# Kernel optimization log

Measured on AMD Instinct MI355X. Metric: run time of the kernel, lower is better.

The kernel has to match this reference:

```python
import jax, jax.numpy as jnp
import numpy as np

KNN, D, CONV_NUM, LEVELS, POOL_RATIO = 4, 64, 6, 3, 8
QN, RFN, NS, H, W = 4, 32, 4, 64, 64
CN = LEVELS * CONV_NUM  # 18 = 3 embed levels x 6 correlation variants


def instance_norm(x, eps=1e-5):
    # InstanceNorm2d(affine=False): normalize each (sample, channel) over H,W (biased var)
    m = x.mean(axis=(-2, -1), keepdims=True)
    v = x.var(axis=(-2, -1), keepdims=True)
    return (x - m) * jax.lax.rsqrt(v + eps)


def conv2d(x, w, b):
    y = jax.lax.conv_general_dilated(x, w, (1, 1), 'SAME', dimension_numbers=('NCHW', 'OIHW', 'NCHW'))
    return y + b[None, :, None, None]


def conv1x1x1(x, w, b):
    # Conv3d kernel 1x1x1 == pure channel mixing; x: (qn,C,ns,h,w), w: (Cout,Cin)
    return jnp.einsum('qcshw,oc->qoshw', x, w) + b[None, :, None, None, None]


def head(x, w1, b1, w2, b2, w3, b3):
    x = jax.nn.relu(conv2d(x, w1, b1))
    x = jax.nn.relu(conv2d(x, w2, b2))
    return conv2d(x, w3, b3)


def setup_inputs():
    key = jax.random.key(0)
    ks = iter(jax.random.split(key, 64))
    def rn(shape, scale=0.05):
        return jax.random.normal(next(ks), shape, jnp.float32) * scale
    inp = {'corr': jax.random.normal(next(ks), (QN, RFN, NS, CN, H, W), jnp.float32)}
    inp['scale_conv_w1'] = rn((D, CN * KNN)); inp['scale_conv_b1'] = rn((D,))
    inp['scale_conv_w2'] = rn((D, D)); inp['scale_conv_b2'] = rn((D,))
    inp['score_conv_w1'] = rn((D, LEVELS * KNN)); inp['score_conv_b1'] = rn((D,))
    inp['score_conv_w2'] = rn((D, D)); inp['score_conv_b2'] = rn((D,))
    for name, cout in (('scale_pred', 1), ('offset_pred', 2), ('score_pred', 1)):
        inp[name + '_w1'] = rn((D, D, 3, 3)); inp[name + '_b1'] = rn((D,))
        inp[name + '_w2'] = rn((D, D, 3, 3)); inp[name + '_b2'] = rn((D,))
        inp[name + '_w3'] = rn((cout, D, 3, 3)); inp[name + '_b3'] = rn((cout,))
    return inp


def _maps(corr, scale_conv_w1, scale_conv_b1, scale_conv_w2, scale_conv_b2,
          score_conv_w1, score_conv_b1, score_conv_w2, score_conv_b2,
          scale_pred_w1, scale_pred_b1, scale_pred_w2, scale_pred_b2, scale_pred_w3, scale_pred_b3,
          offset_pred_w1, offset_pred_b1, offset_pred_w2, offset_pred_b2, offset_pred_w3, offset_pred_b3,
          score_pred_w1, score_pred_b1, score_pred_w2, score_pred_b2, score_pred_w3, score_pred_b3):
    qn, rfn, ns, cn, h, w = corr.shape
    corr_n = instance_norm(corr)                         # score_norm
    # per-(scale,position) matching score per reference -> knn refs
    ref_score = corr_n.mean(axis=3)                      # qn,rfn,ns,h,w
    rs = jnp.moveaxis(ref_score, 1, -1)                  # qn,ns,h,w,rfn
    _, top_idx = jax.lax.top_k(rs, KNN)                  # qn,ns,h,w,knn
    feat = jnp.transpose(corr_n, (0, 2, 4, 5, 1, 3))     # qn,ns,h,w,rfn,cn
    knn_feat = jnp.take_along_axis(feat, top_idx[..., None], axis=4)  # qn,ns,h,w,knn,cn
    x_scale = jnp.transpose(knn_feat.reshape(qn, ns, h, w, KNN * cn), (0, 4, 1, 2, 3))  # qn,72,ns,h,w
    lvl = corr_n.reshape(qn, rfn, ns, LEVELS, CONV_NUM, h, w).mean(axis=4)  # per-level score
    lvl = jnp.transpose(lvl, (0, 2, 4, 5, 1, 3))         # qn,ns,h,w,rfn,3
    knn_lvl = jnp.take_along_axis(lvl, top_idx[..., None], axis=4)
    x_score = jnp.transpose(knn_lvl.reshape(qn, ns, h, w, KNN * LEVELS), (0, 4, 1, 2, 3))  # qn,12,ns,h,w
    xs = conv1x1x1(jax.nn.relu(conv1x1x1(x_scale, scale_conv_w1, scale_conv_b1)), scale_conv_w2, scale_conv_b2).max(axis=2)
    xc = conv1x1x1(jax.nn.relu(conv1x1x1(x_score, score_conv_w1, score_conv_b1)), score_conv_w2, score_conv_b2).max(axis=2)
    scales = head(xs, scale_pred_w1, scale_pred_b1, scale_pred_w2, scale_pred_b2, scale_pred_w3, scale_pred_b3)
    offsets = head(xc, offset_pred_w1, offset_pred_b1, offset_pred_w2, offset_pred_b2, offset_pred_w3, offset_pred_b3)
    scores = head(xc, score_pred_w1, score_pred_b1, score_pred_w2, score_pred_b2, score_pred_w3, score_pred_b3)
    return scores, scales, offsets


def reference(corr, scale_conv_w1, scale_conv_b1, scale_conv_w2, scale_conv_b2,
              score_conv_w1, score_conv_b1, score_conv_w2, score_conv_b2,
              scale_pred_w1, scale_pred_b1, scale_pred_w2, scale_pred_b2, scale_pred_w3, scale_pred_b3,
              offset_pred_w1, offset_pred_b1, offset_pred_w2, offset_pred_b2, offset_pred_w3, offset_pred_b3,
              score_pred_w1, score_pred_b1, score_pred_w2, score_pred_b2, score_pred_w3, score_pred_b3):
    scores, scales, offsets = _maps(corr, scale_conv_w1, scale_conv_b1, scale_conv_w2, scale_conv_b2,
                                    score_conv_w1, score_conv_b1, score_conv_w2, score_conv_b2,
                                    scale_pred_w1, scale_pred_b1, scale_pred_w2, scale_pred_b2, scale_pred_w3, scale_pred_b3,
                                    offset_pred_w1, offset_pred_b1, offset_pred_w2, offset_pred_b2, offset_pred_w3, offset_pred_b3,
                                    score_pred_w1, score_pred_b1, score_pred_w2, score_pred_b2, score_pred_w3, score_pred_b3)
    # parse_detection: argmax + advanced-index gathers
    qn = scores.shape[0]; h, w = scores.shape[-2:]
    sid = jnp.argmax(scores.reshape(qn, -1), axis=1)
    sy, sx = sid // w, sid % w
    q = jnp.arange(qn)
    off = offsets[q, :, sy, sx]                          # qn,2
    pos = (jnp.stack([sx, sy], -1).astype(scores.dtype) + off + 0.5) * POOL_RATIO - 0.5
    scl = 2.0 ** scales[q, 0, sy, sx]
    return pos, scl, scores, scales, offsets
```

## Files before the change

kernel.cpp:

```cpp
#include <hip/hip_runtime.h>

#define HW 4096

__global__ __launch_bounds__(256) void k_stats(const float* __restrict__ corr,
                                               float* __restrict__ scl,
                                               float* __restrict__ shf) {
  int g = blockIdx.x;
  const float4* p = (const float4*)(corr + (size_t)g * HW);
  int t = threadIdx.x;
  float s = 0.f, s2 = 0.f;
#pragma unroll
  for (int i = 0; i < 4; i++) {
    float4 v = p[t + i * 256];
    s += v.x + v.y + v.z + v.w;
    s2 += v.x * v.x + v.y * v.y + v.z * v.z + v.w * v.w;
  }
#pragma unroll
  for (int o = 32; o > 0; o >>= 1) {
    s += __shfl_down(s, o, 64);
    s2 += __shfl_down(s2, o, 64);
  }
  __shared__ float ls[4], ls2[4];
  int wid = t >> 6;
  if ((t & 63) == 0) { ls[wid] = s; ls2[wid] = s2; }
  __syncthreads();
  if (t == 0) {
    float S = ls[0] + ls[1] + ls[2] + ls[3];
    float S2 = ls2[0] + ls2[1] + ls2[2] + ls2[3];
    float m = S * (1.f / HW);
    float var = S2 * (1.f / HW) - m * m;
    float r = rsqrtf(var + 1e-5f);
    scl[g] = r;
    shf[g] = -m * r;
  }
}

__global__ __launch_bounds__(256) void k_wx(
    const float* __restrict__ p0, const float* __restrict__ p1,
    const float* __restrict__ p2, const float* __restrict__ p3,
    const float* __restrict__ p4, const float* __restrict__ p5,
    float* __restrict__ wT, const float* __restrict__ w1s,
    const float* __restrict__ w2s, const float* __restrict__ w1c,
    const float* __restrict__ w2c, float* __restrict__ wm) {
  int b = blockIdx.x;
  int t = threadIdx.x;
  if (b < 96) {
    int arr = b >> 4;
    int chunk = b & 15;
    const float* src = (arr == 0) ? p0
                       : (arr == 1) ? p1
                       : (arr == 2) ? p2
                       : (arr == 3) ? p3
                       : (arr == 4) ? p4 : p5;
    float* dst = wT + arr * 36864;
#pragma unroll
    for (int i = 0; i < 9; i++) {
      int e = chunk * 2304 + i * 256 + t;
      int oc = e / 576;
      int rem = e - oc * 576;
      dst[rem * 64 + oc] = src[e];
    }
  } else {
    int i = (b - 96) * 256 + t;
    if (i < 4608) {
      int c = i >> 6, o = i & 63;
      wm[i] = w1s[o * 72 + c];
    } else if (i < 8704) {
      int j = i - 4608;
      int c = j >> 6, o = j & 63;
      wm[i] = w2s[o * 64 + c];
    } else if (i < 9472) {
      int j = i - 8704;
      int c = j >> 6, o = j & 63;
      wm[i] = w1c[o * 12 + c];
    } else if (i < 13568) {
      int j = i - 9472;
      int c = j >> 6, o = j & 63;
      wm[i] = w2c[o * 64 + c];
    }
  }
}

__global__ __launch_bounds__(256) void k_refscore(const float* __restrict__ corr,
                                                  const float* __restrict__ scl,
                                                  const float* __restrict__ shf,
                                                  float* __restrict__ rs) {
  int b = blockIdx.x;
  int grp = b >> 2;
  int i4 = (b & 3) * 256 + threadIdx.x;
  const float* base = corr + (size_t)grp * 18 * HW;
  float4 acc = make_float4(0.f, 0.f, 0.f, 0.f);
  float sh = 0.f;
#pragma unroll
  for (int c = 0; c < 18; c++) {
    float s = scl[grp * 18 + c];
    sh += shf[grp * 18 + c];
    float4 v = ((const float4*)(base + c * HW))[i4];
    acc.x += v.x * s; acc.y += v.y * s; acc.z += v.z * s; acc.w += v.w * s;
  }
  const float inv = 1.f / 18.f;
  float4 o;
  o.x = (acc.x + sh) * inv; o.y = (acc.y + sh) * inv;
  o.z = (acc.z + sh) * inv; o.w = (acc.w + sh) * inv;
  ((float4*)(rs + (size_t)grp * HW))[i4] = o;
}

__global__ __launch_bounds__(256) void k_topk(const float* __restrict__ rs,
                                              int* __restrict__ topidx) {
  __shared__ float st[32 * 256];
  int b = blockIdx.x;
  int pxc = b & 15;
  int ns = (b >> 4) & 3;
  int q = b >> 6;
  int t = threadIdx.x;
  int pxb = pxc * 256;
#pragma unroll 8
  for (int r = 0; r < 32; r++)
    st[r * 256 + t] = rs[((q * 32 + r) * 4 + ns) * HW + pxb + t];
  __syncthreads();
  float v[32];
#pragma unroll
  for (int r = 0; r < 32; r++) v[r] = st[r * 256 + t];
  unsigned mask = 0;
  int sel[4];
#pragma unroll
  for (int k = 0; k < 4; k++) {
    float best = -3.4e38f;
    int bi = 0;
#pragma unroll
    for (int r = 0; r < 32; r++) {
      bool take = (!(mask & (1u << r))) && (v[r] > best);
      best = take ? v[r] : best;
      bi = take ? r : bi;
    }
    sel[k] = bi;
    mask |= (1u << bi);
  }
  ((int4*)topidx)[(q * 4 + ns) * HW + pxb + t] =
      make_int4(sel[0], sel[1], sel[2], sel[3]);
}

__global__ __launch_bounds__(256) void k_gather(const float* __restrict__ corr,
                                                const float* __restrict__ scl,
                                                const float* __restrict__ shf,
                                                const int* __restrict__ topidx,
                                                float* __restrict__ vbuf) {
  __shared__ float ls[32], lsh[32];
  int b = blockIdx.x;
  int c = b % 18;
  int rest = b / 18;
  int ns = rest & 3;
  int pxc = (rest >> 2) & 15;
  int q = rest >> 6;
  int t = threadIdx.x;
  int px = pxc * 256 + t;

  if (t < 32) {
    int g = q * 2304 + t * 72 + ns * 18 + c;
    ls[t] = scl[g];
    lsh[t] = shf[g];
  }
  int4 ti = ((const int4*)topidx)[(q * 4 + ns) * HW + px];
  int rk0 = ti.x, rk1 = ti.y, rk2 = ti.z, rk3 = ti.w;
  __syncthreads();

  const float* base = corr + (size_t)(((q * 32) * 4 + ns) * 18 + c) * HW + px;
  float v0 = 0.f, v1 = 0.f, v2 = 0.f, v3 = 0.f;
#pragma unroll
  for (int r = 0; r < 32; r++) {
    float x = base[(size_t)r * 72 * HW];
    v0 = (rk0 == r) ? x : v0;
    v1 = (rk1 == r) ? x : v1;
    v2 = (rk2 == r) ? x : v2;
    v3 = (rk3 == r) ? x : v3;
  }
  v0 = v0 * ls[rk0] + lsh[rk0];
  v1 = v1 * ls[rk1] + lsh[rk1];
  v2 = v2 * ls[rk2] + lsh[rk2];
  v3 = v3 * ls[rk3] + lsh[rk3];
  size_t ob = (size_t)((q * 4 + ns) * 72 + c) * HW + px;
  vbuf[ob] = v0;
  vbuf[ob + 18 * HW] = v1;
  vbuf[ob + 36 * HW] = v2;
  vbuf[ob + 54 * HW] = v3;
}

__global__ __launch_bounds__(256) void k_mlps(const float* __restrict__ vbuf,
                                              const float* __restrict__ w1T,
                                              const float* __restrict__ b1,
                                              const float* __restrict__ w2T,
                                              const float* __restrict__ b2,
                                              float* __restrict__ xs) {
  __shared__ float red8[8 * 256];
  int blk = blockIdx.x;
  int q = blk >> 6, pxc = blk & 63;
  int t = threadIdx.x;
  int ns = t >> 6;
  int lane = t & 63;
  int px = pxc * 64 + lane;

  float v[72];
  const float* vb = vbuf + (size_t)((q * 4 + ns) * 72) * HW + px;
#pragma unroll
  for (int j = 0; j < 72; j++) v[j] = vb[(size_t)j * HW];

  float h[64];
#pragma unroll
  for (int o = 0; o < 64; o++) h[o] = b1[o];
#pragma unroll 4
  for (int c = 0; c < 72; c++) {
    float x = v[c];
    const float* wr = w1T + c * 64;
#pragma unroll
    for (int o = 0; o < 64; o++) h[o] = fmaf(wr[o], x, h[o]);
  }
#pragma unroll
  for (int o = 0; o < 64; o++) h[o] = fmaxf(h[o], 0.f);
  float a[64];
#pragma unroll
  for (int o = 0; o < 64; o++) a[o] = b2[o];
#pragma unroll 4
  for (int c = 0; c < 64; c++) {
    float x = h[c];
    const float* wr = w2T + c * 64;
#pragma unroll
    for (int o = 0; o < 64; o++) a[o] = fmaf(wr[o], x, a[o]);
  }
#pragma unroll
  for (int og = 0; og < 8; og++) {
#pragma unroll
    for (int j = 0; j < 8; j++) red8[j * 256 + t] = a[og * 8 + j];
    __syncthreads();
#pragma unroll
    for (int jj = 0; jj < 2; jj++) {
      int j2 = ns * 2 + jj;
      float m = red8[j2 * 256 + lane];
#pragma unroll
      for (int n2 = 1; n2 < 4; n2++)
        m = fmaxf(m, red8[j2 * 256 + n2 * 64 + lane]);
      xs[(size_t)(q * 64 + og * 8 + j2) * HW + px] = m;
    }
    __syncthreads();
  }
}

__global__ __launch_bounds__(256) void k_mlpc(const float* __restrict__ vbuf,
                                              const float* __restrict__ w1T,
                                              const float* __restrict__ b1,
                                              const float* __restrict__ w2T,
                                              const float* __restrict__ b2,
                                              float* __restrict__ xc) {
  __shared__ float red8[8 * 256];
  int blk = blockIdx.x;
  int q = blk >> 6, pxc = blk & 63;
  int t = threadIdx.x;
  int ns = t >> 6;
  int lane = t & 63;
  int px = pxc * 64 + lane;

  float xsc[12];
  const float* vb = vbuf + (size_t)((q * 4 + ns) * 72) * HW + px;
#pragma unroll
  for (int k = 0; k < 4; k++)
#pragma unroll
    for (int l = 0; l < 3; l++) {
      float s = 0.f;
#pragma unroll
      for (int j = 0; j < 6; j++)
        s += vb[(size_t)(k * 18 + l * 6 + j) * HW];
      xsc[k * 3 + l] = s * (1.f / 6.f);
    }
  float h[64];
#pragma unroll
  for (int o = 0; o < 64; o++) h[o] = b1[o];
#pragma unroll 4
  for (int c = 0; c < 12; c++) {
    float x = xsc[c];
    const float* wr = w1T + c * 64;
#pragma unroll
    for (int o = 0; o < 64; o++) h[o] = fmaf(wr[o], x, h[o]);
  }
#pragma unroll
  for (int o = 0; o < 64; o++) h[o] = fmaxf(h[o], 0.f);
  float a[64];
#pragma unroll
  for (int o = 0; o < 64; o++) a[o] = b2[o];
#pragma unroll 4
  for (int c = 0; c < 64; c++) {
    float x = h[c];
    const float* wr = w2T + c * 64;
#pragma unroll
    for (int o = 0; o < 64; o++) a[o] = fmaf(wr[o], x, a[o]);
  }
#pragma unroll
  for (int og = 0; og < 8; og++) {
#pragma unroll
    for (int j = 0; j < 8; j++) red8[j * 256 + t] = a[og * 8 + j];
    __syncthreads();
#pragma unroll
    for (int jj = 0; jj < 2; jj++) {
      int j2 = ns * 2 + jj;
      float m = red8[j2 * 256 + lane];
#pragma unroll
      for (int n2 = 1; n2 < 4; n2++)
        m = fmaxf(m, red8[j2 * 256 + n2 * 64 + lane]);
      xc[(size_t)(q * 64 + og * 8 + j2) * HW + px] = m;
    }
    __syncthreads();
  }
}

template <bool RELU>
__global__ __launch_bounds__(256) void k_conv3h(
    const float* __restrict__ in0, const float* __restrict__ in1,
    const float* __restrict__ in2, const float* __restrict__ w0,
    const float* __restrict__ w1, const float* __restrict__ w2,
    const float* __restrict__ bb0, const float* __restrict__ bb1,
    const float* __restrict__ bb2, float* __restrict__ o0,
    float* __restrict__ o1, float* __restrict__ o2) {
  __shared__ float tile[16 * 10 * 72];
  int b = blockIdx.x;
  int hi = b >> 5;
  int og = hi / 3;
  int head = hi - og * 3;
  int q = (b >> 3) & 3;
  int rt = b & 7;
  const float* in = head == 0 ? in0 : head == 1 ? in1 : in2;
  const float* wT = head == 0 ? w0 : head == 1 ? w1 : w2;
  const float* bb = head == 0 ? bb0 : head == 1 ? bb1 : bb2;
  float* outp = head == 0 ? o0 : head == 1 ? o1 : o2;

  int t = threadIdx.x;
  int w = t & 63;
  int wr = t >> 6;
  int lane4 = t & 15;
  int rgrp = t >> 4;
  float acc[2][8];
#pragma unroll
  for (int pr = 0; pr < 2; pr++)
#pragma unroll
    for (int o = 0; o < 8; o++) acc[pr][o] = 0.f;
  const float* inq = in + (size_t)q * 64 * HW;

  for (int icc = 0; icc < 4; icc++) {
    __syncthreads();
    if (t < 160) { tile[t * 72 + 3] = 0.f; tile[t * 72 + 68] = 0.f; }
#pragma unroll
    for (int p = 0; p < 10; p++) {
      int idx = p * 16 + rgrp;
      int ch = idx / 10;
      int r = idx - ch * 10;
      int grow = rt * 8 + r - 1;
      float4 val = make_float4(0.f, 0.f, 0.f, 0.f);
      if (grow >= 0 && grow < 64)
        val = *(const float4*)(inq + (size_t)(icc * 16 + ch) * HW + grow * 64 +
                               lane4 * 4);
      *(float4*)(tile + idx * 72 + 4 + lane4 * 4) = val;
    }
    __syncthreads();
#pragma unroll 2
    for (int ic = 0; ic < 16; ic++) {
      float xv[4][3];
      const float* tb = tile + (ic * 10 + wr * 2) * 72 + w + 3;
#pragma unroll
      for (int rr = 0; rr < 4; rr++)
#pragma unroll
        for (int dc = 0; dc < 3; dc++) xv[rr][dc] = tb[rr * 72 + dc];
      const float* wb = wT + (size_t)(icc * 16 + ic) * 9 * 64 + og * 8;
#pragma unroll
      for (int dr = 0; dr < 3; dr++)
#pragma unroll
        for (int dc = 0; dc < 3; dc++) {
          const float* wv = wb + (dr * 3 + dc) * 64;
#pragma unroll
          for (int o = 0; o < 8; o++) {
            float wj = wv[o];
            acc[0][o] = fmaf(wj, xv[0 + dr][dc], acc[0][o]);
            acc[1][o] = fmaf(wj, xv[1 + dr][dc], acc[1][o]);
          }
        }
    }
  }
#pragma unroll
  for (int pr = 0; pr < 2; pr++) {
    int orow = rt * 8 + wr * 2 + pr;
#pragma unroll
    for (int o = 0; o < 8; o++) {
      float rz = acc[pr][o] + bb[og * 8 + o];
      if (RELU) rz = fmaxf(rz, 0.f);
      outp[((size_t)q * 64 + og * 8 + o) * HW + orow * 64 + w] = rz;
    }
  }
}

__global__ __launch_bounds__(256) void k_convSh(
    const float* __restrict__ in0, const float* __restrict__ in1,
    const float* __restrict__ in2, const float* __restrict__ wt0,
    const float* __restrict__ wt1, const float* __restrict__ wt2,
    const float* __restrict__ bb0, const float* __restrict__ bb1,
    const float* __restrict__ bb2, float* __restrict__ o0,
    float* __restrict__ o1, float* __restrict__ o2) {
  __shared__ float tile[64 * 3 * 66];
  __shared__ float red[4 * 2 * 64];
  int b = blockIdx.x;
  int head = b >> 8;
  int q = (b >> 6) & 3;
  int row = b & 63;
  const float* in = head == 0 ? in0 : head == 1 ? in1 : in2;
  const float* wt = head == 0 ? wt0 : head == 1 ? wt1 : wt2;
  const float* bb = head == 0 ? bb0 : head == 1 ? bb1 : bb2;
  float* outp = head == 0 ? o0 : head == 1 ? o1 : o2;
  int noc = (head == 1) ? 2 : 1;

  int t = threadIdx.x;
  int w = t & 63;
  int sub = t >> 6;
  if (t < 192) { tile[t * 66] = 0.f; tile[t * 66 + 65] = 0.f; }
  __syncthreads();
  const float* inq = in + (size_t)q * 64 * HW;
#pragma unroll
  for (int i = 0; i < 48; i++) {
    int idx = i * 4 + sub;
    int ic = idx / 3;
    int r = idx - ic * 3;
    int grow = row + r - 1;
    float val = 0.f;
    if (grow >= 0 && grow < 64) val = inq[(size_t)ic * HW + grow * 64 + w];
    tile[idx * 66 + 1 + w] = val;
  }
  __syncthreads();
  float acc0 = 0.f, acc1 = 0.f;
#pragma unroll 4
  for (int i = 0; i < 16; i++) {
    int ic = sub * 16 + i;
    float x[9];
#pragma unroll
    for (int dr = 0; dr < 3; dr++)
#pragma unroll
      for (int dc = 0; dc < 3; dc++)
        x[dr * 3 + dc] = tile[(ic * 3 + dr) * 66 + w + dc];
    const float* wb = wt + (size_t)ic * 9;
#pragma unroll
    for (int j = 0; j < 9; j++) acc0 += wb[j] * x[j];
    if (noc == 2) {
      const float* wb1 = wt + 576 + (size_t)ic * 9;
#pragma unroll
      for (int j = 0; j < 9; j++) acc1 += wb1[j] * x[j];
    }
  }
  red[(sub * 2 + 0) * 64 + w] = acc0;
  if (noc == 2) red[(sub * 2 + 1) * 64 + w] = acc1;
  __syncthreads();
  if (t < 128) {
    int o = t >> 6;
    if (o < noc) {
      float s = red[(0 * 2 + o) * 64 + w] + red[(1 * 2 + o) * 64 + w] +
                red[(2 * 2 + o) * 64 + w] + red[(3 * 2 + o) * 64 + w] + bb[o];
      outp[((size_t)q * noc + o) * HW + row * 64 + w] = s;
    }
  }
}

__global__ __launch_bounds__(256) void k_final(const float* __restrict__ scores,
                                               const float* __restrict__ scales,
                                               const float* __restrict__ offsets,
                                               float* __restrict__ pos,
                                               float* __restrict__ sclo) {
  int q = blockIdx.x, t = threadIdx.x;
  float best = -3.4e38f;
  int bi = 1 << 30;
  for (int i = t; i < HW; i += 256) {
    float v = scores[q * HW + i];
    if (v > best) { best = v; bi = i; }
  }
  __shared__ float bv[256];
  __shared__ int bix[256];
  bv[t] = best;
  bix[t] = bi;
  __syncthreads();
  for (int s = 128; s > 0; s >>= 1) {
    if (t < s) {
      if (bv[t + s] > bv[t] || (bv[t + s] == bv[t] && bix[t + s] < bix[t])) {
        bv[t] = bv[t + s];
        bix[t] = bix[t + s];
      }
    }
    __syncthreads();
  }
  if (t == 0) {
    int sid = bix[0];
    int sy = sid >> 6, sx = sid & 63;
    float o0 = offsets[(q * 2 + 0) * HW + sid];
    float o1 = offsets[(q * 2 + 1) * HW + sid];
    pos[q * 2 + 0] = ((float)sx + o0 + 0.5f) * 8.f - 0.5f;
    pos[q * 2 + 1] = ((float)sy + o1 + 0.5f) * 8.f - 0.5f;
    sclo[q] = exp2f(scales[q * HW + sid]);
  }
}

extern "C" void kernel_launch(void* const* d_in, const int* in_sizes, int n_in,
                              void* d_out, int out_size, void* d_ws, size_t ws_size,
                              hipStream_t stream) {
  const float* corr = (const float*)d_in[0];
  const float* w1s = (const float*)d_in[1];
  const float* b1s = (const float*)d_in[2];
  const float* w2s = (const float*)d_in[3];
  const float* b2s = (const float*)d_in[4];
  const float* w1c = (const float*)d_in[5];
  const float* b1c = (const float*)d_in[6];
  const float* w2c = (const float*)d_in[7];
  const float* b2c = (const float*)d_in[8];

  float* out = (float*)d_out;
  float* pos = out;
  float* sclo = out + 8;
  float* scores = out + 12;
  float* scales = out + 12 + 16384;
  float* offsets = out + 12 + 32768;

  char* ws = (char*)d_ws;
  float* st_scl = (float*)(ws + 0);
  float* st_shf = (float*)(ws + 36864);
  int* topidx = (int*)(ws + 73728);
  float* rs = (float*)(ws + 1122304);
  float* vbuf = rs;
  float* wT = (float*)(ws + 19996672);
  float* wmT = (float*)(ws + 20881408);
  float* xs = (float*)(ws + 20971520);
  float* xc = (float*)(ws + 25165824);
  float* t1s = vbuf;
  float* t1o = (float*)((char*)vbuf + 4194304);
  float* t1c = (float*)((char*)vbuf + 8388608);
  float* t2c = (float*)((char*)vbuf + 12582912);
  float* t2s = xs;
  float* t2o = xc;

  k_wx<<<149, 256, 0, stream>>>((const float*)d_in[9], (const float*)d_in[11],
                                (const float*)d_in[15], (const float*)d_in[17],
                                (const float*)d_in[21], (const float*)d_in[23],
                                wT, w1s, w2s, w1c, w2c, wmT);
  k_stats<<<9216, 256, 0, stream>>>(corr, st_scl, st_shf);
  k_refscore<<<2048, 256, 0, stream>>>(corr, st_scl, st_shf, rs);
  k_topk<<<256, 256, 0, stream>>>(rs, topidx);
  k_gather<<<4608, 256, 0, stream>>>(corr, st_scl, st_shf, topidx, vbuf);
  k_mlps<<<256, 256, 0, stream>>>(vbuf, wmT, b1s, wmT + 4608, b2s, xs);
  k_mlpc<<<256, 256, 0, stream>>>(vbuf, wmT + 8704, b1c, wmT + 9472, b2c, xc);
  k_conv3h<true><<<768, 256, 0, stream>>>(
      xs, xc, xc, wT, wT + 2 * 36864, wT + 4 * 36864,
      (const float*)d_in[10], (const float*)d_in[16], (const float*)d_in[22],
      t1s, t1o, t1c);
  k_conv3h<true><<<768, 256, 0, stream>>>(
      t1s, t1o, t1c, wT + 1 * 36864, wT + 3 * 36864, wT + 5 * 36864,
      (const float*)d_in[12], (const float*)d_in[18], (const float*)d_in[24],
      t2s, t2o, t2c);
  k_convSh<<<768, 256, 0, stream>>>(
      t2s, t2o, t2c, (const float*)d_in[13], (const float*)d_in[19],
      (const float*)d_in[25], (const float*)d_in[14], (const float*)d_in[20],
      (const float*)d_in[26], scales, offsets, scores);

  k_final<<<4, 256, 0, stream>>>(scores, scales, offsets, pos, sclo);
}
```

Before: 549.8 us.

## Fuse gather with both MLPs, merge stats with weight prep, widen conv channel tiles

The top-k gather, the scale MLP and the score MLP now run as one kernel, so the gathered 72-channel buffer no longer makes a round trip through global memory and corr is read into registers per pixel. The stats kernel and the weight-transpose kernel are merged into a single launch. The 3x3 conv kernel now computes 16 output channels per thread instead of 8, on half as many blocks. In exchange, the fused kernel streams all of corr from only 256 register-heavy blocks at one block per CU, which may leave too few waves to hide memory latency. The conv change also lowers the block count and raises register pressure.

```diff
diff --git a/kernel.cpp b/kernel.cpp
--- a/kernel.cpp
+++ b/kernel.cpp
@@ -2,48 +2,47 @@
 
 #define HW 4096
 
-__global__ __launch_bounds__(256) void k_stats(const float* __restrict__ corr,
-                                               float* __restrict__ scl,
-                                               float* __restrict__ shf) {
-  int g = blockIdx.x;
-  const float4* p = (const float4*)(corr + (size_t)g * HW);
-  int t = threadIdx.x;
-  float s = 0.f, s2 = 0.f;
-#pragma unroll
-  for (int i = 0; i < 4; i++) {
-    float4 v = p[t + i * 256];
-    s += v.x + v.y + v.z + v.w;
-    s2 += v.x * v.x + v.y * v.y + v.z * v.z + v.w * v.w;
-  }
-#pragma unroll
-  for (int o = 32; o > 0; o >>= 1) {
-    s += __shfl_down(s, o, 64);
-    s2 += __shfl_down(s2, o, 64);
-  }
-  __shared__ float ls[4], ls2[4];
-  int wid = t >> 6;
-  if ((t & 63) == 0) { ls[wid] = s; ls2[wid] = s2; }
-  __syncthreads();
-  if (t == 0) {
-    float S = ls[0] + ls[1] + ls[2] + ls[3];
-    float S2 = ls2[0] + ls2[1] + ls2[2] + ls2[3];
-    float m = S * (1.f / HW);
-    float var = S2 * (1.f / HW) - m * m;
-    float r = rsqrtf(var + 1e-5f);
-    scl[g] = r;
-    shf[g] = -m * r;
-  }
-}
-
-__global__ __launch_bounds__(256) void k_wx(
+__global__ __launch_bounds__(256) void k_stats_wx(
+    const float* __restrict__ corr, float* __restrict__ scl,
+    float* __restrict__ shf,
     const float* __restrict__ p0, const float* __restrict__ p1,
     const float* __restrict__ p2, const float* __restrict__ p3,
     const float* __restrict__ p4, const float* __restrict__ p5,
     float* __restrict__ wT, const float* __restrict__ w1s,
     const float* __restrict__ w2s, const float* __restrict__ w1c,
     const float* __restrict__ w2c, float* __restrict__ wm) {
-  int b = blockIdx.x;
   int t = threadIdx.x;
+  if (blockIdx.x < 9216) {
+    int g = blockIdx.x;
+    const float4* p = (const float4*)(corr + (size_t)g * HW);
+    float s = 0.f, s2 = 0.f;
+#pragma unroll
+    for (int i = 0; i < 4; i++) {
+      float4 v = p[t + i * 256];
+      s += v.x + v.y + v.z + v.w;
+      s2 += v.x * v.x + v.y * v.y + v.z * v.z + v.w * v.w;
+    }
+#pragma unroll
+    for (int o = 32; o > 0; o >>= 1) {
+      s += __shfl_down(s, o, 64);
+      s2 += __shfl_down(s2, o, 64);
+    }
+    __shared__ float ls[4], ls2[4];
+    int wid = t >> 6;
+    if ((t & 63) == 0) { ls[wid] = s; ls2[wid] = s2; }
+    __syncthreads();
+    if (t == 0) {
+      float S = ls[0] + ls[1] + ls[2] + ls[3];
+      float S2 = ls2[0] + ls2[1] + ls2[2] + ls2[3];
+      float m = S * (1.f / HW);
+      float var = S2 * (1.f / HW) - m * m;
+      float r = rsqrtf(var + 1e-5f);
+      scl[g] = r;
+      shf[g] = -m * r;
+    }
+    return;
+  }
+  int b = blockIdx.x - 9216;
   if (b < 96) {
     int arr = b >> 4;
     int chunk = b & 15;
@@ -140,57 +139,37 @@
       make_int4(sel[0], sel[1], sel[2], sel[3]);
 }
 
-__global__ __launch_bounds__(256) void k_gather(const float* __restrict__ corr,
-                                                const float* __restrict__ scl,
-                                                const float* __restrict__ shf,
-                                                const int* __restrict__ topidx,
-                                                float* __restrict__ vbuf) {
-  __shared__ float ls[32], lsh[32];
-  int b = blockIdx.x;
-  int c = b % 18;
-  int rest = b / 18;
-  int ns = rest & 3;
-  int pxc = (rest >> 2) & 15;
-  int q = rest >> 6;
-  int t = threadIdx.x;
-  int px = pxc * 256 + t;
-
-  if (t < 32) {
-    int g = q * 2304 + t * 72 + ns * 18 + c;
-    ls[t] = scl[g];
-    lsh[t] = shf[g];
-  }
-  int4 ti = ((const int4*)topidx)[(q * 4 + ns) * HW + px];
-  int rk0 = ti.x, rk1 = ti.y, rk2 = ti.z, rk3 = ti.w;
-  __syncthreads();
-
-  const float* base = corr + (size_t)(((q * 32) * 4 + ns) * 18 + c) * HW + px;
-  float v0 = 0.f, v1 = 0.f, v2 = 0.f, v3 = 0.f;
-#pragma unroll
-  for (int r = 0; r < 32; r++) {
-    float x = base[(size_t)r * 72 * HW];
-    v0 = (rk0 == r) ? x : v0;
-    v1 = (rk1 == r) ? x : v1;
-    v2 = (rk2 == r) ? x : v2;
-    v3 = (rk3 == r) ? x : v3;
-  }
-  v0 = v0 * ls[rk0] + lsh[rk0];
-  v1 = v1 * ls[rk1] + lsh[rk1];
-  v2 = v2 * ls[rk2] + lsh[rk2];
-  v3 = v3 * ls[rk3] + lsh[rk3];
-  size_t ob = (size_t)((q * 4 + ns) * 72 + c) * HW + px;
-  vbuf[ob] = v0;
-  vbuf[ob + 18 * HW] = v1;
-  vbuf[ob + 36 * HW] = v2;
-  vbuf[ob + 54 * HW] = v3;
-}
-
-__global__ __launch_bounds__(256) void k_mlps(const float* __restrict__ vbuf,
-                                              const float* __restrict__ w1T,
-                                              const float* __restrict__ b1,
-                                              const float* __restrict__ w2T,
-                                              const float* __restrict__ b2,
-                                              float* __restrict__ xs) {
+#define L1GRP(VV, OFF)                                        \
+  _Pragma("unroll") for (int c = 0; c < 18; c++) {            \
+    const float* wr = wm + (OFF + c) * 64;                    \
+    float x = VV[c];                                          \
+    _Pragma("unroll") for (int o = 0; o < 64; o++)            \
+        h[o] = fmaf(wr[o], x, h[o]);                          \
+  }
+
+#define NSMAX_STORE(OUTP)                                     \
+  _Pragma("unroll") for (int og = 0; og < 8; og++) {          \
+    _Pragma("unroll") for (int j = 0; j < 8; j++)             \
+        red8[j * 256 + t] = a[og * 8 + j];                    \
+    __syncthreads();                                          \
+    _Pragma("unroll") for (int jj = 0; jj < 2; jj++) {        \
+      int j2 = ns * 2 + jj;                                   \
+      float m = red8[j2 * 256 + lane];                        \
+      _Pragma("unroll") for (int n2 = 1; n2 < 4; n2++)        \
+          m = fmaxf(m, red8[j2 * 256 + n2 * 64 + lane]);      \
+      OUTP[(size_t)(q * 64 + og * 8 + j2) * HW + px] = m;     \
+    }                                                         \
+    __syncthreads();                                          \
+  }
+
+__global__ __launch_bounds__(256, 1) void k_gmlp(
+    const float* __restrict__ corr, const float* __restrict__ scl,
+    const float* __restrict__ shf, const int* __restrict__ topidx,
+    const float* __restrict__ wm, const float* __restrict__ b1s,
+    const float* __restrict__ b2s, const float* __restrict__ b1c,
+    const float* __restrict__ b2c, float* __restrict__ xs,
+    float* __restrict__ xc) {
+  __shared__ float lscl[2304], lshf[2304];
   __shared__ float red8[8 * 256];
   int blk = blockIdx.x;
   int q = blk >> 6, pxc = blk & 63;
@@ -199,115 +178,97 @@
   int lane = t & 63;
   int px = pxc * 64 + lane;
 
-  float v[72];
-  const float* vb = vbuf + (size_t)((q * 4 + ns) * 72) * HW + px;
-#pragma unroll
-  for (int j = 0; j < 72; j++) v[j] = vb[(size_t)j * HW];
+  for (int i = t; i < 2304; i += 256) {
+    lscl[i] = scl[q * 2304 + i];
+    lshf[i] = shf[q * 2304 + i];
+  }
+  int4 ti = ((const int4*)topidx)[(q * 4 + ns) * HW + px];
+  __syncthreads();
+  int rk0 = ti.x, rk1 = ti.y, rk2 = ti.z, rk3 = ti.w;
+
+  float v0[18], v1[18], v2[18], v3[18];
+#pragma unroll
+  for (int c = 0; c < 18; c++) { v0[c] = 0.f; v1[c] = 0.f; v2[c] = 0.f; v3[c] = 0.f; }
+  const float* cb = corr + ((size_t)((q * 32) * 4 + ns) * 18) * HW + px;
+#pragma unroll 2
+  for (int r = 0; r < 32; r++) {
+    const float* br = cb + (size_t)r * (72 * HW);
+    bool m0 = (r == rk0), m1 = (r == rk1), m2 = (r == rk2), m3 = (r == rk3);
+#pragma unroll
+    for (int c = 0; c < 18; c++) {
+      float x = br[c * HW];
+      v0[c] = m0 ? x : v0[c];
+      v1[c] = m1 ? x : v1[c];
+      v2[c] = m2 ? x : v2[c];
+      v3[c] = m3 ? x : v3[c];
+    }
+  }
+  int e0 = rk0 * 72 + ns * 18, e1 = rk1 * 72 + ns * 18;
+  int e2 = rk2 * 72 + ns * 18, e3 = rk3 * 72 + ns * 18;
+#pragma unroll
+  for (int c = 0; c < 18; c++) {
+    v0[c] = fmaf(v0[c], lscl[e0 + c], lshf[e0 + c]);
+    v1[c] = fmaf(v1[c], lscl[e1 + c], lshf[e1 + c]);
+    v2[c] = fmaf(v2[c], lscl[e2 + c], lshf[e2 + c]);
+    v3[c] = fmaf(v3[c], lscl[e3 + c], lshf[e3 + c]);
+  }
+  float xsc[12];
+#pragma unroll
+  for (int l = 0; l < 3; l++) {
+    float s0 = 0.f, s1 = 0.f, s2 = 0.f, s3 = 0.f;
+#pragma unroll
+    for (int j = 0; j < 6; j++) {
+      s0 += v0[l * 6 + j]; s1 += v1[l * 6 + j];
+      s2 += v2[l * 6 + j]; s3 += v3[l * 6 + j];
+    }
+    xsc[0 + l] = s0 * (1.f / 6.f);
+    xsc[3 + l] = s1 * (1.f / 6.f);
+    xsc[6 + l] = s2 * (1.f / 6.f);
+    xsc[9 + l] = s3 * (1.f / 6.f);
+  }
 
   float h[64];
 #pragma unroll
-  for (int o = 0; o < 64; o++) h[o] = b1[o];
-#pragma unroll 4
-  for (int c = 0; c < 72; c++) {
-    float x = v[c];
-    const float* wr = w1T + c * 64;
-#pragma unroll
-    for (int o = 0; o < 64; o++) h[o] = fmaf(wr[o], x, h[o]);
-  }
+  for (int o = 0; o < 64; o++) h[o] = b1s[o];
+  L1GRP(v0, 0)
+  L1GRP(v1, 18)
+  L1GRP(v2, 36)
+  L1GRP(v3, 54)
 #pragma unroll
   for (int o = 0; o < 64; o++) h[o] = fmaxf(h[o], 0.f);
   float a[64];
 #pragma unroll
-  for (int o = 0; o < 64; o++) a[o] = b2[o];
-#pragma unroll 4
+  for (int o = 0; o < 64; o++) a[o] = b2s[o];
+#pragma unroll
   for (int c = 0; c < 64; c++) {
+    const float* wr = wm + 4608 + c * 64;
     float x = h[c];
-    const float* wr = w2T + c * 64;
 #pragma unroll
     for (int o = 0; o < 64; o++) a[o] = fmaf(wr[o], x, a[o]);
   }
-#pragma unroll
-  for (int og = 0; og < 8; og++) {
-#pragma unroll
-    for (int j = 0; j < 8; j++) red8[j * 256 + t] = a[og * 8 + j];
-    __syncthreads();
-#pragma unroll
-    for (int jj = 0; jj < 2; jj++) {
-      int j2 = ns * 2 + jj;
-      float m = red8[j2 * 256 + lane];
-#pragma unroll
-      for (int n2 = 1; n2 < 4; n2++)
-        m = fmaxf(m, red8[j2 * 256 + n2 * 64 + lane]);
-      xs[(size_t)(q * 64 + og * 8 + j2) * HW + px] = m;
-    }
-    __syncthreads();
-  }
-}
-
-__global__ __launch_bounds__(256) void k_mlpc(const float* __restrict__ vbuf,
-                                              const float* __restrict__ w1T,
-                                              const float* __restrict__ b1,
-                                              const float* __restrict__ w2T,
-                                              const float* __restrict__ b2,
-                                              float* __restrict__ xc) {
-  __shared__ float red8[8 * 256];
-  int blk = blockIdx.x;
-  int q = blk >> 6, pxc = blk & 63;
-  int t = threadIdx.x;
-  int ns = t >> 6;
-  int lane = t & 63;
-  int px = pxc * 64 + lane;
-
-  float xsc[12];
-  const float* vb = vbuf + (size_t)((q * 4 + ns) * 72) * HW + px;
-#pragma unroll
-  for (int k = 0; k < 4; k++)
-#pragma unroll
-    for (int l = 0; l < 3; l++) {
-      float s = 0.f;
-#pragma unroll
-      for (int j = 0; j < 6; j++)
-        s += vb[(size_t)(k * 18 + l * 6 + j) * HW];
-      xsc[k * 3 + l] = s * (1.f / 6.f);
-    }
-  float h[64];
-#pragma unroll
-  for (int o = 0; o < 64; o++) h[o] = b1[o];
-#pragma unroll 4
+  NSMAX_STORE(xs)
+
+#pragma unroll
+  for (int o = 0; o < 64; o++) h[o] = b1c[o];
+#pragma unroll
   for (int c = 0; c < 12; c++) {
+    const float* wr = wm + 8704 + c * 64;
     float x = xsc[c];
-    const float* wr = w1T + c * 64;
 #pragma unroll
     for (int o = 0; o < 64; o++) h[o] = fmaf(wr[o], x, h[o]);
   }
 #pragma unroll
   for (int o = 0; o < 64; o++) h[o] = fmaxf(h[o], 0.f);
-  float a[64];
-#pragma unroll
-  for (int o = 0; o < 64; o++) a[o] = b2[o];
-#pragma unroll 4
+#pragma unroll
+  for (int o = 0; o < 64; o++) a[o] = b2c[o];
+#pragma unroll
   for (int c = 0; c < 64; c++) {
+    const float* wr = wm + 9472 + c * 64;
     float x = h[c];
-    const float* wr = w2T + c * 64;
 #pragma unroll
     for (int o = 0; o < 64; o++) a[o] = fmaf(wr[o], x, a[o]);
   }
-#pragma unroll
-  for (int og = 0; og < 8; og++) {
-#pragma unroll
-    for (int j = 0; j < 8; j++) red8[j * 256 + t] = a[og * 8 + j];
-    __syncthreads();
-#pragma unroll
-    for (int jj = 0; jj < 2; jj++) {
-      int j2 = ns * 2 + jj;
-      float m = red8[j2 * 256 + lane];
-#pragma unroll
-      for (int n2 = 1; n2 < 4; n2++)
-        m = fmaxf(m, red8[j2 * 256 + n2 * 64 + lane]);
-      xc[(size_t)(q * 64 + og * 8 + j2) * HW + px] = m;
-    }
-    __syncthreads();
-  }
+  NSMAX_STORE(xc)
 }
 
 template <bool RELU>
@@ -335,11 +296,11 @@
   int wr = t >> 6;
   int lane4 = t & 15;
   int rgrp = t >> 4;
-  float acc[2][8];
+  float acc[2][16];
 #pragma unroll
   for (int pr = 0; pr < 2; pr++)
 #pragma unroll
-    for (int o = 0; o < 8; o++) acc[pr][o] = 0.f;
+    for (int o = 0; o < 16; o++) acc[pr][o] = 0.f;
   const float* inq = in + (size_t)q * 64 * HW;
 
   for (int icc = 0; icc < 4; icc++) {
@@ -366,14 +327,14 @@
       for (int rr = 0; rr < 4; rr++)
 #pragma unroll
         for (int dc = 0; dc < 3; dc++) xv[rr][dc] = tb[rr * 72 + dc];
-      const float* wb = wT + (size_t)(icc * 16 + ic) * 9 * 64 + og * 8;
+      const float* wb = wT + (size_t)(icc * 16 + ic) * 9 * 64 + og * 16;
 #pragma unroll
       for (int dr = 0; dr < 3; dr++)
 #pragma unroll
         for (int dc = 0; dc < 3; dc++) {
           const float* wv = wb + (dr * 3 + dc) * 64;
 #pragma unroll
-          for (int o = 0; o < 8; o++) {
+          for (int o = 0; o < 16; o++) {
             float wj = wv[o];
             acc[0][o] = fmaf(wj, xv[0 + dr][dc], acc[0][o]);
             acc[1][o] = fmaf(wj, xv[1 + dr][dc], acc[1][o]);
@@ -385,10 +346,10 @@
   for (int pr = 0; pr < 2; pr++) {
     int orow = rt * 8 + wr * 2 + pr;
 #pragma unroll
-    for (int o = 0; o < 8; o++) {
-      float rz = acc[pr][o] + bb[og * 8 + o];
+    for (int o = 0; o < 16; o++) {
+      float rz = acc[pr][o] + bb[og * 16 + o];
       if (RELU) rz = fmaxf(rz, 0.f);
-      outp[((size_t)q * 64 + og * 8 + o) * HW + orow * 64 + w] = rz;
+      outp[((size_t)q * 64 + og * 16 + o) * HW + orow * 64 + w] = rz;
     }
   }
 }
@@ -523,33 +484,30 @@
   float* st_shf = (float*)(ws + 36864);
   int* topidx = (int*)(ws + 73728);
   float* rs = (float*)(ws + 1122304);
-  float* vbuf = rs;
   float* wT = (float*)(ws + 19996672);
   float* wmT = (float*)(ws + 20881408);
   float* xs = (float*)(ws + 20971520);
   float* xc = (float*)(ws + 25165824);
-  float* t1s = vbuf;
-  float* t1o = (float*)((char*)vbuf + 4194304);
-  float* t1c = (float*)((char*)vbuf + 8388608);
-  float* t2c = (float*)((char*)vbuf + 12582912);
+  float* t1s = rs;
+  float* t1o = (float*)((char*)rs + 4194304);
+  float* t1c = (float*)((char*)rs + 8388608);
+  float* t2c = (float*)((char*)rs + 12582912);
   float* t2s = xs;
   float* t2o = xc;
 
-  k_wx<<<149, 256, 0, stream>>>((const float*)d_in[9], (const float*)d_in[11],
-                                (const float*)d_in[15], (const float*)d_in[17],
-                                (const float*)d_in[21], (const float*)d_in[23],
-                                wT, w1s, w2s, w1c, w2c, wmT);
-  k_stats<<<9216, 256, 0, stream>>>(corr, st_scl, st_shf);
+  k_stats_wx<<<9365, 256, 0, stream>>>(
+      corr, st_scl, st_shf, (const float*)d_in[9], (const float*)d_in[11],
+      (const float*)d_in[15], (const float*)d_in[17], (const float*)d_in[21],
+      (const float*)d_in[23], wT, w1s, w2s, w1c, w2c, wmT);
   k_refscore<<<2048, 256, 0, stream>>>(corr, st_scl, st_shf, rs);
   k_topk<<<256, 256, 0, stream>>>(rs, topidx);
-  k_gather<<<4608, 256, 0, stream>>>(corr, st_scl, st_shf, topidx, vbuf);
-  k_mlps<<<256, 256, 0, stream>>>(vbuf, wmT, b1s, wmT + 4608, b2s, xs);
-  k_mlpc<<<256, 256, 0, stream>>>(vbuf, wmT + 8704, b1c, wmT + 9472, b2c, xc);
-  k_conv3h<true><<<768, 256, 0, stream>>>(
+  k_gmlp<<<256, 256, 0, stream>>>(corr, st_scl, st_shf, topidx, wmT, b1s, b2s,
+                                  b1c, b2c, xs, xc);
+  k_conv3h<true><<<384, 256, 0, stream>>>(
       xs, xc, xc, wT, wT + 2 * 36864, wT + 4 * 36864,
       (const float*)d_in[10], (const float*)d_in[16], (const float*)d_in[22],
       t1s, t1o, t1c);
-  k_conv3h<true><<<768, 256, 0, stream>>>(
+  k_conv3h<true><<<384, 256, 0, stream>>>(
       t1s, t1o, t1c, wT + 1 * 36864, wT + 3 * 36864, wT + 5 * 36864,
       (const float*)d_in[12], (const float*)d_in[18], (const float*)d_in[24],
       t2s, t2o, t2c);
```

New measurement: 750.9 us. 36.6% more time.
